# Optimization experiments

Measured on AMD Instinct MI355X. Metric: run time of the kernel, lower is better.

The kernel has to match this reference:

```python
import jax, jax.numpy as jnp
import numpy as np

B, S, D, H, F, L = 4, 2048, 768, 12, 3072, 4
DH = D // H  # dim_head = 64
EPS = 1e-5


def _layernorm(x, g, b):
    mu = jnp.mean(x, axis=-1, keepdims=True)
    var = jnp.var(x, axis=-1, keepdims=True)
    return (x - mu) * jax.lax.rsqrt(var + EPS) * g + b


def setup_inputs() -> dict:
    key = jax.random.key(0)
    ks = jax.random.split(key, 12)
    sc = 0.02
    x = jax.random.normal(ks[0], (B, S, D), dtype=jnp.float32)
    # causal mask: True where attention is disallowed (j > i)
    causal = jnp.triu(jnp.ones((S, S), dtype=bool), k=1)
    attn_mask = jnp.broadcast_to(causal, (B, S, S))
    Wq = jax.random.normal(ks[1], (L, D, D), dtype=jnp.float32) * sc
    Wk = jax.random.normal(ks[2], (L, D, D), dtype=jnp.float32) * sc
    Wv = jax.random.normal(ks[3], (L, D, D), dtype=jnp.float32) * sc
    Wo = jax.random.normal(ks[4], (L, D, D), dtype=jnp.float32) * sc
    bo = jnp.zeros((L, D), dtype=jnp.float32)
    ln1_g = jnp.ones((L, D), dtype=jnp.float32)
    ln1_b = jnp.zeros((L, D), dtype=jnp.float32)
    W1 = jax.random.normal(ks[5], (L, D, F), dtype=jnp.float32) * sc
    b1 = jnp.zeros((L, F), dtype=jnp.float32)
    W2 = jax.random.normal(ks[6], (L, F, D), dtype=jnp.float32) * sc
    b2 = jnp.zeros((L, D), dtype=jnp.float32)
    ln2_g = jnp.ones((L, D), dtype=jnp.float32)
    ln2_b = jnp.zeros((L, D), dtype=jnp.float32)
    return dict(x=x, attn_mask=attn_mask, Wq=Wq, Wk=Wk, Wv=Wv, Wo=Wo, bo=bo,
                ln1_g=ln1_g, ln1_b=ln1_b, W1=W1, b1=b1, W2=W2, b2=b2,
                ln2_g=ln2_g, ln2_b=ln2_b)


def _decoder_layer(x, mask, Wq, Wk, Wv, Wo, bo, ln1_g, ln1_b, W1, b1, W2, b2, ln2_g, ln2_b):
    # multi-head attention (dropout = identity in eval)
    q = (x @ Wq).reshape(B, S, H, DH).transpose(0, 2, 1, 3)  # (B,H,S,DH)
    k = (x @ Wk).reshape(B, S, H, DH).transpose(0, 2, 1, 3)
    v = (x @ Wv).reshape(B, S, H, DH).transpose(0, 2, 1, 3)
    a = jnp.einsum('bhqd,bhkd->bhqk', q, k) / jnp.sqrt(jnp.float32(DH))
    a = jnp.where(mask[:, None, :, :], jnp.float32(-1e9), a)
    p = jax.nn.softmax(a, axis=-1)
    av = jnp.einsum('bhqk,bhkd->bhqd', p, v)
    av = av.transpose(0, 2, 1, 3).reshape(B, S, D)
    attn_out = av @ Wo + bo
    h = _layernorm(x + attn_out, ln1_g, ln1_b)
    # FFN: Conv1d(kernel=1) == pointwise linear; exact GELU (torch F.gelu default)
    f = jax.nn.gelu(h @ W1 + b1, approximate=False) @ W2 + b2
    return _layernorm(h + f, ln2_g, ln2_b)


def reference(x, attn_mask, Wq, Wk, Wv, Wo, bo, ln1_g, ln1_b, W1, b1, W2, b2, ln2_g, ln2_b):
    for l in range(L):
        x = _decoder_layer(x, attn_mask, Wq[l], Wk[l], Wv[l], Wo[l], bo[l],
                           ln1_g[l], ln1_b[l], W1[l], b1[l], W2[l], b2[l],
                           ln2_g[l], ln2_b[l])
    return x
```

## Files before the change

kernel.cpp:

```cpp
#include <hip/hip_runtime.h>
#include <hip/hip_bf16.h>
#include <math.h>

#define BB 4
#define SS 2048
#define DD 768
#define HH 12
#define DHD 64
#define FF 3072
#define LL 4

typedef float ffrag __attribute__((ext_vector_type(4)));
typedef __bf16 bf16x8 __attribute__((ext_vector_type(8)));
typedef __bf16 bf16x4 __attribute__((ext_vector_type(4)));

__device__ __forceinline__ void gld_lds16(const __bf16* g, __bf16* l) {
  __builtin_amdgcn_global_load_lds(
      (const __attribute__((address_space(1))) void*)g,
      (__attribute__((address_space(3))) void*)l, 16, 0, 0);
}

__device__ __forceinline__ float gelu_f(float x) {
  const float x2 = x * x;
  const float e = __expf(x * fmaf(-0.0713548162f, x2, -1.5957691216f));
  return x / (1.f + e);
}

template <int SWAP>
__device__ __forceinline__ void gemm_core(
    const __bf16* __restrict__ A, const __bf16* __restrict__ Bt,
    __bf16* As, __bf16* Bs, int m0, int n0, int K, int kbeg, int kend,
    int lane, int wid, ffrag (&acc)[4][4]) {
  const int kr = lane >> 4;
  const int ml = lane & 15;
  const int wm = (wid >> 1) * 64;
  const int wn = (wid & 1) * 64;
  for (int k0 = kbeg; k0 < kend; k0 += 64) {
    __syncthreads();
#pragma unroll
    for (int it = 0; it < 4; ++it) {
      const int gidx = it * 256 + wid * 64 + lane;
      const int row = gidx >> 3;
      const int gl = (gidx & 7) ^ (row & 7);
      gld_lds16(A + (size_t)(m0 + row) * K + k0 + gl * 8,
                As + (size_t)(it * 256 + wid * 64) * 8);
      gld_lds16(Bt + (size_t)(n0 + row) * K + k0 + gl * 8,
                Bs + (size_t)(it * 256 + wid * 64) * 8);
    }
    __syncthreads();
#pragma unroll
    for (int kh = 0; kh < 2; ++kh) {
      const int gb = kh * 4 + kr;
      bf16x8 af[4], bfr[4];
#pragma unroll
      for (int i = 0; i < 4; ++i) {
        const int ra = wm + i * 16 + ml;
        af[i] = *(const bf16x8*)(As + ra * 64 + ((gb ^ (ra & 7)) * 8));
        const int rb = wn + i * 16 + ml;
        bfr[i] = *(const bf16x8*)(Bs + rb * 64 + ((gb ^ (rb & 7)) * 8));
      }
#pragma unroll
      for (int i = 0; i < 4; ++i)
#pragma unroll
        for (int j = 0; j < 4; ++j) {
          if (SWAP)
            acc[i][j] = __builtin_amdgcn_mfma_f32_16x16x32_bf16(
                bfr[j], af[i], acc[i][j], 0, 0, 0);
          else
            acc[i][j] = __builtin_amdgcn_mfma_f32_16x16x32_bf16(
                af[i], bfr[j], acc[i][j], 0, 0, 0);
        }
    }
  }
}

template <int ACT, int WRITE_BF16, int SPLITK>
__global__ __launch_bounds__(256) void gemm_std(
    const __bf16* __restrict__ A, const __bf16* __restrict__ Bt,
    const float* __restrict__ bias, float* __restrict__ Cf,
    __bf16* __restrict__ Cb, int M, int N, int K) {
  __shared__ __bf16 As[128 * 64];
  __shared__ __bf16 Bs[128 * 64];
  const int tid = threadIdx.x;
  const int lane = tid & 63;
  const int wid = tid >> 6;
  const int m0 = blockIdx.y * 128;
  const int n0 = blockIdx.x * 128;
  const int wm = (wid >> 1) * 64;
  const int wn = (wid & 1) * 64;
  const int ml = lane & 15;
  const int quad = lane >> 4;

  int kbeg = 0, kend = K;
  if (SPLITK) {
    const int z = blockIdx.z;
    const int half = K >> 1;
    kbeg = z * half;
    kend = kbeg + half;
    Cf += (size_t)z * M * N;
    if (z) bias = nullptr;
  }

  ffrag acc[4][4];
#pragma unroll
  for (int i = 0; i < 4; ++i)
#pragma unroll
    for (int j = 0; j < 4; ++j) acc[i][j] = (ffrag)0.f;

  gemm_core<1>(A, Bt, As, Bs, m0, n0, K, kbeg, kend, lane, wid, acc);

#pragma unroll
  for (int j = 0; j < 4; ++j) {
    const int ncol = n0 + wn + j * 16 + quad * 4;
    float4 b4 = make_float4(0.f, 0.f, 0.f, 0.f);
    if (bias) b4 = *(const float4*)(bias + ncol);
#pragma unroll
    for (int i = 0; i < 4; ++i) {
      const int mrow = m0 + wm + i * 16 + ml;
      float v0 = acc[i][j][0] + b4.x;
      float v1 = acc[i][j][1] + b4.y;
      float v2 = acc[i][j][2] + b4.z;
      float v3 = acc[i][j][3] + b4.w;
      if (ACT) {
        v0 = gelu_f(v0); v1 = gelu_f(v1);
        v2 = gelu_f(v2); v3 = gelu_f(v3);
      }
      if (WRITE_BF16) {
        bf16x4 pk;
        pk[0] = (__bf16)v0; pk[1] = (__bf16)v1;
        pk[2] = (__bf16)v2; pk[3] = (__bf16)v3;
        *(bf16x4*)(Cb + (size_t)mrow * N + ncol) = pk;
      } else {
        float4 o; o.x = v0; o.y = v1; o.z = v2; o.w = v3;
        *(float4*)(Cf + (size_t)mrow * N + ncol) = o;
      }
    }
  }
}

__global__ __launch_bounds__(256) void gemm_qkv(
    const __bf16* __restrict__ A, const __bf16* __restrict__ Bt,
    __bf16* __restrict__ QKb, __bf16* __restrict__ Vt, int M, int K) {
  __shared__ __bf16 As[128 * 64];
  __shared__ __bf16 Bs[128 * 64];
  const int tid = threadIdx.x;
  const int lane = tid & 63;
  const int wid = tid >> 6;
  const int m0 = blockIdx.y * 128;
  const int n0 = blockIdx.x * 128;
  const int wm = (wid >> 1) * 64;
  const int wn = (wid & 1) * 64;
  const int ml = lane & 15;
  const int quad = lane >> 4;

  ffrag acc[4][4];
#pragma unroll
  for (int i = 0; i < 4; ++i)
#pragma unroll
    for (int j = 0; j < 4; ++j) acc[i][j] = (ffrag)0.f;

  if (n0 < 1536) {
    gemm_core<1>(A, Bt, As, Bs, m0, n0, K, 0, K, lane, wid, acc);
#pragma unroll
    for (int j = 0; j < 4; ++j) {
      const int ncol = n0 + wn + j * 16 + quad * 4;
#pragma unroll
      for (int i = 0; i < 4; ++i) {
        const int mrow = m0 + wm + i * 16 + ml;
        bf16x4 pk;
#pragma unroll
        for (int r = 0; r < 4; ++r) pk[r] = (__bf16)acc[i][j][r];
        *(bf16x4*)(QKb + (size_t)mrow * 1536 + ncol) = pk;
      }
    }
  } else {
    gemm_core<0>(A, Bt, As, Bs, m0, n0, K, 0, K, lane, wid, acc);
#pragma unroll
    for (int j = 0; j < 4; ++j) {
      const int vcol = n0 - 1536 + wn + j * 16 + ml;
      const int hh = vcol >> 6, d = vcol & 63;
#pragma unroll
      for (int i = 0; i < 4; ++i) {
        const int row = m0 + wm + i * 16 + quad * 4;
        const int bi = row >> 11, s = row & 2047;
        bf16x4 pk;
#pragma unroll
        for (int r = 0; r < 4; ++r) pk[r] = (__bf16)acc[i][j][r];
        *(bf16x4*)(Vt + ((size_t)(bi * HH + hh) * DHD + d) * SS + s) = pk;
      }
    }
  }
}

__global__ __launch_bounds__(256) void wtrans_kernel(
    const float* __restrict__ src, __bf16* __restrict__ dst, int R, int C,
    size_t src_ls, size_t dst_ls) {
  __shared__ float t[32][33];
  src += (size_t)blockIdx.z * src_ls;
  dst += (size_t)blockIdx.z * dst_ls;
  const int tx = threadIdx.x & 31;
  const int ty = threadIdx.x >> 5;
  const int r0 = blockIdx.y * 32;
  const int c0 = blockIdx.x * 32;
#pragma unroll
  for (int i = 0; i < 4; ++i)
    t[ty + i * 8][tx] = src[(size_t)(r0 + ty + i * 8) * C + c0 + tx];
  __syncthreads();
#pragma unroll
  for (int i = 0; i < 4; ++i)
    dst[(size_t)(c0 + ty + i * 8) * R + r0 + tx] = (__bf16)t[tx][ty + i * 8];
}

__global__ __launch_bounds__(256) void cvt_kernel(
    const float* __restrict__ x, __bf16* __restrict__ y, int n4) {
  const int i = blockIdx.x * 256 + threadIdx.x;
  if (i < n4) {
    const float4 v = *(const float4*)(x + (size_t)i * 4);
    bf16x4 o;
    o[0] = (__bf16)v.x; o[1] = (__bf16)v.y;
    o[2] = (__bf16)v.z; o[3] = (__bf16)v.w;
    *(bf16x4*)(y + (size_t)i * 4) = o;
  }
}

__global__ __launch_bounds__(256, 3) void attn_mfma(
    const __bf16* __restrict__ QK, const __bf16* __restrict__ VT,
    __bf16* __restrict__ O) {
  __shared__ __bf16 qs[64 * 64];
  __shared__ __bf16 ks[2][64 * 64];
  __shared__ __bf16 vts[2][64 * 64];
  __shared__ __bf16 ps[64 * 72];

  const int flat = (int)blockIdx.x + 16 * ((int)blockIdx.y + 12 * (int)blockIdx.z);
  const int sw = (flat & 7) * 96 + (flat >> 3);
  const int xq = sw & 15;
  const int bh = sw >> 4;
  const int h = bh % HH;
  const int b = bh / HH;

  const int tid = threadIdx.x;
  const int lane = tid & 63;
  const int wid = tid >> 6;
  const int ml = lane & 15;
  const int quad = lane >> 4;
  const int wq = wid * 16;
  const size_t rowbase = (size_t)b * SS;
  const int hc = h * 64;
  const size_t vbase = (size_t)(b * HH + h) * DHD;
  const int NT = SS / 64;

  const int gidx0 = wid * 64 + lane;
  const int row0 = gidx0 >> 3;
  const int gl0 = (gidx0 & 7) ^ (row0 & 7);
  const int gidx1 = 256 + wid * 64 + lane;
  const int row1 = gidx1 >> 3;
  const int gl1 = (gidx1 & 7) ^ (row1 & 7);

  for (int ph = 0; ph < 2; ++ph) {
    const int qt = ph ? (NT - 1 - xq) : xq;
    const int q0 = qt * 64;

    __syncthreads();

    gld_lds16(QK + (rowbase + q0 + row0) * 1536 + hc + gl0 * 8,
              qs + (size_t)(wid * 64) * 8);
    gld_lds16(QK + (rowbase + q0 + row1) * 1536 + hc + gl1 * 8,
              qs + (size_t)(256 + wid * 64) * 8);
    gld_lds16(QK + (rowbase + row0) * 1536 + 768 + hc + gl0 * 8,
              ks[0] + (size_t)(wid * 64) * 8);
    gld_lds16(QK + (rowbase + row1) * 1536 + 768 + hc + gl1 * 8,
              ks[0] + (size_t)(256 + wid * 64) * 8);
    gld_lds16(VT + (vbase + row0) * SS + gl0 * 8, vts[0] + (size_t)(wid * 64) * 8);
    gld_lds16(VT + (vbase + row1) * SS + gl1 * 8, vts[0] + (size_t)(256 + wid * 64) * 8);

    ffrag oacc[4];
#pragma unroll
    for (int d = 0; d < 4; ++d) oacc[d] = (ffrag)0.f;
    float l_acc = 0.f;

    for (int ch = 0; ch <= qt; ++ch) {
      const int j0 = ch * 64;
      const int cur = ch & 1;
      __syncthreads();

      if (ch < qt) {
        const int jn = j0 + 64;
        gld_lds16(QK + (rowbase + jn + row0) * 1536 + 768 + hc + gl0 * 8,
                  ks[cur ^ 1] + (size_t)(wid * 64) * 8);
        gld_lds16(QK + (rowbase + jn + row1) * 1536 + 768 + hc + gl1 * 8,
                  ks[cur ^ 1] + (size_t)(256 + wid * 64) * 8);
        gld_lds16(VT + (vbase + row0) * SS + jn + gl0 * 8,
                  vts[cur ^ 1] + (size_t)(wid * 64) * 8);
        gld_lds16(VT + (vbase + row1) * SS + jn + gl1 * 8,
                  vts[cur ^ 1] + (size_t)(256 + wid * 64) * 8);
      }

      ffrag sa[4];
#pragma unroll
      for (int jt = 0; jt < 4; ++jt) sa[jt] = (ffrag)0.f;
#pragma unroll
      for (int kk = 0; kk < 2; ++kk) {
        const int gb = kk * 4 + quad;
        const int ra = wq + ml;
        const bf16x8 qf = *(const bf16x8*)(qs + ra * 64 + ((gb ^ (ra & 7)) * 8));
#pragma unroll
        for (int jt = 0; jt < 4; ++jt) {
          const int rb = jt * 16 + ml;
          const bf16x8 kf =
              *(const bf16x8*)(ks[cur] + rb * 64 + ((gb ^ (rb & 7)) * 8));
          sa[jt] = __builtin_amdgcn_mfma_f32_16x16x32_bf16(kf, qf, sa[jt], 0, 0, 0);
        }
      }

      const bool maskch = (j0 == q0);
      const int qrel = wq + ml;
      float lsum = 0.f;
      bf16x4 pk[4];
#pragma unroll
      for (int jt = 0; jt < 4; ++jt) {
#pragma unroll
        for (int r = 0; r < 4; ++r) {
          float p = __expf(sa[jt][r] * 0.125f);
          if (maskch && (jt * 16 + quad * 4 + r > qrel)) p = 0.f;
          lsum += p;
          pk[jt][r] = (__bf16)p;
        }
      }
      lsum += __shfl_xor(lsum, 16);
      lsum += __shfl_xor(lsum, 32);
      l_acc += lsum;

#pragma unroll
      for (int jt = 0; jt < 4; ++jt)
        *(bf16x4*)(ps + (size_t)(wq + ml) * 72 + jt * 16 + quad * 4) = pk[jt];

#pragma unroll
      for (int kk = 0; kk < 2; ++kk) {
        const bf16x8 ap =
            *(const bf16x8*)(ps + (size_t)(wq + ml) * 72 + kk * 32 + quad * 8);
        const int gb = kk * 4 + quad;
#pragma unroll
        for (int d = 0; d < 4; ++d) {
          const int rv = d * 16 + ml;
          const bf16x8 bv =
              *(const bf16x8*)(vts[cur] + rv * 64 + ((gb ^ (rv & 7)) * 8));
          oacc[d] = __builtin_amdgcn_mfma_f32_16x16x32_bf16(ap, bv, oacc[d], 0, 0, 0);
        }
      }
    }

#pragma unroll
    for (int r = 0; r < 4; ++r) {
      const int qloc = quad * 4 + r;
      const float lr = __shfl(l_acc, qloc);
      const float inv = 1.f / lr;
      const size_t row = rowbase + q0 + wq + qloc;
#pragma unroll
      for (int d = 0; d < 4; ++d)
        O[row * DD + hc + d * 16 + ml] = (__bf16)(oacc[d][r] * inv);
    }
  }
}

__global__ __launch_bounds__(256) void add_ln_kernel(
    const __bf16* __restrict__ X, const float* __restrict__ R1,
    const float* __restrict__ R2, const float* __restrict__ g,
    const float* __restrict__ be, float* __restrict__ Ofp,
    __bf16* __restrict__ Ob) {
  const int row = blockIdx.x * 4 + (threadIdx.x >> 6);
  const int lane = threadIdx.x & 63;
  const __bf16* xr = X + (size_t)row * DD;
  const float* r1 = R1 + (size_t)row * DD;
  const float* r2 = R2 ? R2 + (size_t)row * DD : nullptr;
  float v[12];
  float sum = 0.f;
#pragma unroll
  for (int i = 0; i < 3; ++i) {
    const int c = i * 256 + lane * 4;
    const bf16x4 a = *(const bf16x4*)(xr + c);
    const float4 b = *(const float4*)(r1 + c);
    float4 c2 = make_float4(0.f, 0.f, 0.f, 0.f);
    if (r2) c2 = *(const float4*)(r2 + c);
    v[i * 4 + 0] = (float)a[0] + b.x + c2.x;
    v[i * 4 + 1] = (float)a[1] + b.y + c2.y;
    v[i * 4 + 2] = (float)a[2] + b.z + c2.z;
    v[i * 4 + 3] = (float)a[3] + b.w + c2.w;
    sum += v[i * 4 + 0] + v[i * 4 + 1] + v[i * 4 + 2] + v[i * 4 + 3];
  }
#pragma unroll
  for (int off = 32; off >= 1; off >>= 1) sum += __shfl_xor(sum, off);
  const float mean = sum * (1.f / 768.f);
  float sq = 0.f;
#pragma unroll
  for (int i = 0; i < 12; ++i) {
    const float d = v[i] - mean;
    sq += d * d;
  }
#pragma unroll
  for (int off = 32; off >= 1; off >>= 1) sq += __shfl_xor(sq, off);
  const float inv = rsqrtf(sq * (1.f / 768.f) + 1e-5f);
#pragma unroll
  for (int i = 0; i < 3; ++i) {
    const int c = i * 256 + lane * 4;
    const float4 gg = *(const float4*)(g + c);
    const float4 bb = *(const float4*)(be + c);
    float4 o;
    o.x = (v[i * 4 + 0] - mean) * inv * gg.x + bb.x;
    o.y = (v[i * 4 + 1] - mean) * inv * gg.y + bb.y;
    o.z = (v[i * 4 + 2] - mean) * inv * gg.z + bb.z;
    o.w = (v[i * 4 + 3] - mean) * inv * gg.w + bb.w;
    if (Ofp) *(float4*)(Ofp + (size_t)row * DD + c) = o;
    if (Ob) {
      bf16x4 ob;
      ob[0] = (__bf16)o.x; ob[1] = (__bf16)o.y;
      ob[2] = (__bf16)o.z; ob[3] = (__bf16)o.w;
      *(bf16x4*)(Ob + (size_t)row * DD + c) = ob;
    }
  }
}

extern "C" void kernel_launch(void* const* d_in, const int* in_sizes, int n_in,
                              void* d_out, int out_size, void* d_ws,
                              size_t ws_size, hipStream_t stream) {
  const float* x0   = (const float*)d_in[0];
  const float* Wq   = (const float*)d_in[2];
  const float* Wk   = (const float*)d_in[3];
  const float* Wv   = (const float*)d_in[4];
  const float* Wo   = (const float*)d_in[5];
  const float* bo   = (const float*)d_in[6];
  const float* ln1g = (const float*)d_in[7];
  const float* ln1b = (const float*)d_in[8];
  const float* W1   = (const float*)d_in[9];
  const float* b1   = (const float*)d_in[10];
  const float* W2   = (const float*)d_in[11];
  const float* b2   = (const float*)d_in[12];
  const float* ln2g = (const float*)d_in[13];
  const float* ln2b = (const float*)d_in[14];

  float* out = (float*)d_out;

  const size_t NTD = (size_t)BB * SS * DD;
  __bf16* qkbf = (__bf16*)d_ws;
  __bf16* vtbf = qkbf + (size_t)BB * SS * 1536;
  __bf16* btbf = vtbf + NTD;
  __bf16* midbf = qkbf;
  __bf16* hbf  = btbf + NTD;
  float* aw    = (float*)(hbf + NTD);
  __bf16* wT   = (__bf16*)(aw + 2 * NTD);
  __bf16* xbf  = (__bf16*)d_out;

  const size_t WTL = 7077888;
  const size_t OQK = 0, OWO = (size_t)2304 * 768, OW1 = 2359296, OW2 = 4718592;

  const int M = BB * SS;
  const size_t DSQ = (size_t)DD * DD;

  cvt_kernel<<<(int)(NTD / 4 + 255) / 256, 256, 0, stream>>>(x0, xbf, (int)(NTD / 4));

  wtrans_kernel<<<dim3(24, 24, LL), 256, 0, stream>>>(Wq, wT + OQK, DD, DD, DSQ, WTL);
  wtrans_kernel<<<dim3(24, 24, LL), 256, 0, stream>>>(Wk, wT + (size_t)768 * 768, DD, DD, DSQ, WTL);
  wtrans_kernel<<<dim3(24, 24, LL), 256, 0, stream>>>(Wv, wT + (size_t)1536 * 768, DD, DD, DSQ, WTL);
  wtrans_kernel<<<dim3(24, 24, LL), 256, 0, stream>>>(Wo, wT + OWO, DD, DD, DSQ, WTL);
  wtrans_kernel<<<dim3(96, 24, LL), 256, 0, stream>>>(W1, wT + OW1, DD, FF, (size_t)DD * FF, WTL);
  wtrans_kernel<<<dim3(24, 96, LL), 256, 0, stream>>>(W2, wT + OW2, FF, DD, (size_t)FF * DD, WTL);

  for (int l = 0; l < LL; ++l) {
    const float* bol = bo + (size_t)l * DD;
    const float* g1 = ln1g + (size_t)l * DD;
    const float* be1 = ln1b + (size_t)l * DD;
    const float* b1l = b1 + (size_t)l * FF;
    const float* b2l = b2 + (size_t)l * DD;
    const float* g2 = ln2g + (size_t)l * DD;
    const float* be2 = ln2b + (size_t)l * DD;
    __bf16* wqkvT = wT + l * WTL + OQK;
    __bf16* woT   = wT + l * WTL + OWO;
    __bf16* w1T   = wT + l * WTL + OW1;
    __bf16* w2T   = wT + l * WTL + OW2;
    const bool last = (l == LL - 1);

    gemm_qkv<<<dim3(18, 64), 256, 0, stream>>>(xbf, wqkvT, qkbf, vtbf, M, DD);
    attn_mfma<<<dim3(SS / 128, HH, BB), 256, 0, stream>>>(qkbf, vtbf, btbf);
    gemm_std<0, 0, 0><<<dim3(6, 64), 256, 0, stream>>>(
        btbf, woT, bol, aw, nullptr, M, DD, DD);
    add_ln_kernel<<<M / 4, 256, 0, stream>>>(
        xbf, aw, nullptr, g1, be1, nullptr, hbf);
    gemm_std<1, 1, 0><<<dim3(24, 64), 256, 0, stream>>>(
        hbf, w1T, b1l, nullptr, midbf, M, FF, DD);
    gemm_std<0, 0, 1><<<dim3(6, 64, 2), 256, 0, stream>>>(
        midbf, w2T, b2l, aw, nullptr, M, DD, FF);
    add_ln_kernel<<<M / 4, 256, 0, stream>>>(
        hbf, aw, aw + NTD, g2, be2, last ? out : nullptr, last ? nullptr : xbf);
  }
}
```

Measured before the change: 1.208 ms.

## Add triple-buffered 256x128 FFN1 GEMM and XCD-aware block swizzle

Adds a new 512-thread GEMM kernel for the FFN up-projection with 256x128 tiles and a three-stage LDS pipeline driven by explicit vmcnt waits. It uses direct global-to-LDS loads and raises MFMA priority during compute, aiming to hide load latency. All GEMMs also remap block indices so neighbouring tiles land on the same XCD, which should improve L2 reuse. The larger LDS footprint (about 144KB) may limit occupancy to one block per CU.

```diff
diff --git a/kernel.cpp b/kernel.cpp
--- a/kernel.cpp
+++ b/kernel.cpp
@@ -24,6 +24,10 @@
   const float x2 = x * x;
   const float e = __expf(x * fmaf(-0.0713548162f, x2, -1.5957691216f));
   return x / (1.f + e);
+}
+
+__device__ __forceinline__ int xcd_swz(int flat, int nwg) {
+  return (flat & 7) * (nwg >> 3) + (flat >> 3);
 }
 
 template <int SWAP>
@@ -84,8 +88,13 @@
   const int tid = threadIdx.x;
   const int lane = tid & 63;
   const int wid = tid >> 6;
-  const int m0 = blockIdx.y * 128;
-  const int n0 = blockIdx.x * 128;
+  const int nx = (int)gridDim.x, ny = (int)gridDim.y, nz = (int)gridDim.z;
+  const int flat = (int)blockIdx.x + nx * ((int)blockIdx.y + ny * (int)blockIdx.z);
+  const int sw = xcd_swz(flat, nx * ny * nz);
+  const int m0 = (sw % ny) * 128;
+  const int r = sw / ny;
+  const int n0 = (r % nx) * 128;
+  const int z = r / nx;
   const int wm = (wid >> 1) * 64;
   const int wn = (wid & 1) * 64;
   const int ml = lane & 15;
@@ -93,7 +102,6 @@
 
   int kbeg = 0, kend = K;
   if (SPLITK) {
-    const int z = blockIdx.z;
     const int half = K >> 1;
     kbeg = z * half;
     kend = kbeg + half;
@@ -138,6 +146,122 @@
   }
 }
 
+__device__ __forceinline__ void stage3(const __bf16* A, const __bf16* Bt,
+                                       __bf16* as, __bf16* bs, int K, int k0,
+                                       int tid, int wid) {
+#pragma unroll
+  for (int it = 0; it < 4; ++it) {
+    const int gidx = it * 512 + tid;
+    const int row = gidx >> 3;
+    const int gl = (gidx & 7) ^ (row & 7);
+    gld_lds16(A + (size_t)row * K + k0 + gl * 8,
+              as + (size_t)(it * 512 + wid * 64) * 8);
+  }
+#pragma unroll
+  for (int it = 0; it < 2; ++it) {
+    const int gidx = it * 512 + tid;
+    const int row = gidx >> 3;
+    const int gl = (gidx & 7) ^ (row & 7);
+    gld_lds16(Bt + (size_t)row * K + k0 + gl * 8,
+              bs + (size_t)(it * 512 + wid * 64) * 8);
+  }
+}
+
+template <int ACT>
+__global__ __launch_bounds__(512) void gemm3s(
+    const __bf16* __restrict__ A, const __bf16* __restrict__ Bt,
+    const float* __restrict__ bias, __bf16* __restrict__ Cb,
+    int M, int N, int K) {
+  __shared__ __bf16 As[3][256 * 64];
+  __shared__ __bf16 Bs[3][128 * 64];
+  const int tid = threadIdx.x;
+  const int lane = tid & 63;
+  const int wid = tid >> 6;
+  const int nx = N >> 7;
+  const int ny = M >> 8;
+  const int flat = (int)blockIdx.x + nx * (int)blockIdx.y;
+  const int sw = xcd_swz(flat, nx * ny);
+  const int m0 = (sw % ny) * 256;
+  const int n0 = (sw / ny) * 128;
+  const __bf16* Ab = A + (size_t)m0 * K;
+  const __bf16* Bb = Bt + (size_t)n0 * K;
+  const int ml = lane & 15;
+  const int kr = lane >> 4;
+  const int quad = kr;
+  const int wm = (wid >> 1) * 64;
+  const int wn = (wid & 1) * 64;
+
+  ffrag acc[4][4];
+#pragma unroll
+  for (int i = 0; i < 4; ++i)
+#pragma unroll
+    for (int j = 0; j < 4; ++j) acc[i][j] = (ffrag)0.f;
+
+  const int nt = K >> 6;
+  stage3(Ab, Bb, As[0], Bs[0], K, 0, tid, wid);
+  if (nt > 1) stage3(Ab, Bb, As[1], Bs[1], K, 64, tid, wid);
+
+  for (int t = 0; t < nt; ++t) {
+    const int s = t % 3;
+    if (t + 2 < nt)
+      stage3(Ab, Bb, As[(t + 2) % 3], Bs[(t + 2) % 3], K, (t + 2) * 64, tid, wid);
+    if (t + 2 < nt)
+      asm volatile("s_waitcnt vmcnt(12)" ::: "memory");
+    else if (t + 1 < nt)
+      asm volatile("s_waitcnt vmcnt(6)" ::: "memory");
+    else
+      asm volatile("s_waitcnt vmcnt(0)" ::: "memory");
+    __builtin_amdgcn_s_barrier();
+    const __bf16* as = As[s];
+    const __bf16* bs = Bs[s];
+#pragma unroll
+    for (int kh = 0; kh < 2; ++kh) {
+      const int gb = kh * 4 + kr;
+      bf16x8 af[4], bfr[4];
+#pragma unroll
+      for (int i = 0; i < 4; ++i) {
+        const int ra = wm + i * 16 + ml;
+        af[i] = *(const bf16x8*)(as + ra * 64 + ((gb ^ (ra & 7)) * 8));
+        const int rb = wn + i * 16 + ml;
+        bfr[i] = *(const bf16x8*)(bs + rb * 64 + ((gb ^ (rb & 7)) * 8));
+      }
+      __builtin_amdgcn_s_setprio(1);
+#pragma unroll
+      for (int i = 0; i < 4; ++i)
+#pragma unroll
+        for (int j = 0; j < 4; ++j)
+          acc[i][j] = __builtin_amdgcn_mfma_f32_16x16x32_bf16(
+              bfr[j], af[i], acc[i][j], 0, 0, 0);
+      __builtin_amdgcn_s_setprio(0);
+    }
+    asm volatile("s_waitcnt lgkmcnt(0)" ::: "memory");
+    __builtin_amdgcn_s_barrier();
+  }
+
+#pragma unroll
+  for (int j = 0; j < 4; ++j) {
+    const int ncol = n0 + wn + j * 16 + quad * 4;
+    float4 b4 = make_float4(0.f, 0.f, 0.f, 0.f);
+    if (bias) b4 = *(const float4*)(bias + ncol);
+#pragma unroll
+    for (int i = 0; i < 4; ++i) {
+      const int mrow = m0 + wm + i * 16 + ml;
+      float v0 = acc[i][j][0] + b4.x;
+      float v1 = acc[i][j][1] + b4.y;
+      float v2 = acc[i][j][2] + b4.z;
+      float v3 = acc[i][j][3] + b4.w;
+      if (ACT) {
+        v0 = gelu_f(v0); v1 = gelu_f(v1);
+        v2 = gelu_f(v2); v3 = gelu_f(v3);
+      }
+      bf16x4 pk;
+      pk[0] = (__bf16)v0; pk[1] = (__bf16)v1;
+      pk[2] = (__bf16)v2; pk[3] = (__bf16)v3;
+      *(bf16x4*)(Cb + (size_t)mrow * N + ncol) = pk;
+    }
+  }
+}
+
 __global__ __launch_bounds__(256) void gemm_qkv(
     const __bf16* __restrict__ A, const __bf16* __restrict__ Bt,
     __bf16* __restrict__ QKb, __bf16* __restrict__ Vt, int M, int K) {
@@ -146,8 +270,11 @@
   const int tid = threadIdx.x;
   const int lane = tid & 63;
   const int wid = tid >> 6;
-  const int m0 = blockIdx.y * 128;
-  const int n0 = blockIdx.x * 128;
+  const int nx = (int)gridDim.x, ny = (int)gridDim.y;
+  const int flat = (int)blockIdx.x + nx * (int)blockIdx.y;
+  const int sw = xcd_swz(flat, nx * ny);
+  const int m0 = (sw % ny) * 128;
+  const int n0 = (sw / ny) * 128;
   const int wm = (wid >> 1) * 64;
   const int wn = (wid & 1) * 64;
   const int ml = lane & 15;
@@ -484,8 +611,8 @@
         btbf, woT, bol, aw, nullptr, M, DD, DD);
     add_ln_kernel<<<M / 4, 256, 0, stream>>>(
         xbf, aw, nullptr, g1, be1, nullptr, hbf);
-    gemm_std<1, 1, 0><<<dim3(24, 64), 256, 0, stream>>>(
-        hbf, w1T, b1l, nullptr, midbf, M, FF, DD);
+    gemm3s<1><<<dim3(FF / 128, M / 256), 512, 0, stream>>>(
+        hbf, w1T, b1l, midbf, M, FF, DD);
     gemm_std<0, 0, 1><<<dim3(6, 64, 2), 256, 0, stream>>>(
         midbf, w2T, b2l, aw, nullptr, M, DD, FF);
     add_ln_kernel<<<M / 4, 256, 0, stream>>>(
```

Result: slower. 1.319 ms (+9.1%).

## Double-buffer GEMM LDS tiles, raise MFMA priority, swizzle blocks across XCDs

Applied to the files above, without the earlier changes.

The GEMM core now double-buffers its shared-memory tiles. It issues the global-to-LDS loads for the next K tile before running the MFMAs on the current one, which removes the second barrier per iteration and overlaps load latency with compute. MFMA sections are wrapped in s_setprio, and the block index is remapped with an XCD-aware swizzle so neighbouring tiles land on the same XCD and share its L2. In exchange, LDS use per block doubles to 64KB, which can lower occupancy.

```diff
diff --git a/kernel.cpp b/kernel.cpp
--- a/kernel.cpp
+++ b/kernel.cpp
@@ -24,6 +24,26 @@
   const float x2 = x * x;
   const float e = __expf(x * fmaf(-0.0713548162f, x2, -1.5957691216f));
   return x / (1.f + e);
+}
+
+__device__ __forceinline__ int xcd_swz(int flat, int nwg) {
+  return (flat & 7) * (nwg >> 3) + (flat >> 3);
+}
+
+__device__ __forceinline__ void stage_tile(
+    const __bf16* __restrict__ A, const __bf16* __restrict__ Bt,
+    __bf16* As, __bf16* Bs, int m0, int n0, int K, int k0,
+    int lane, int wid) {
+#pragma unroll
+  for (int it = 0; it < 4; ++it) {
+    const int gidx = it * 256 + wid * 64 + lane;
+    const int row = gidx >> 3;
+    const int gl = (gidx & 7) ^ (row & 7);
+    gld_lds16(A + (size_t)(m0 + row) * K + k0 + gl * 8,
+              As + (size_t)(it * 256 + wid * 64) * 8);
+    gld_lds16(Bt + (size_t)(n0 + row) * K + k0 + gl * 8,
+              Bs + (size_t)(it * 256 + wid * 64) * 8);
+  }
 }
 
 template <int SWAP>
@@ -35,19 +55,16 @@
   const int ml = lane & 15;
   const int wm = (wid >> 1) * 64;
   const int wn = (wid & 1) * 64;
+
+  stage_tile(A, Bt, As, Bs, m0, n0, K, kbeg, lane, wid);
+  int cur = 0;
   for (int k0 = kbeg; k0 < kend; k0 += 64) {
     __syncthreads();
-#pragma unroll
-    for (int it = 0; it < 4; ++it) {
-      const int gidx = it * 256 + wid * 64 + lane;
-      const int row = gidx >> 3;
-      const int gl = (gidx & 7) ^ (row & 7);
-      gld_lds16(A + (size_t)(m0 + row) * K + k0 + gl * 8,
-                As + (size_t)(it * 256 + wid * 64) * 8);
-      gld_lds16(Bt + (size_t)(n0 + row) * K + k0 + gl * 8,
-                Bs + (size_t)(it * 256 + wid * 64) * 8);
-    }
-    __syncthreads();
+    if (k0 + 64 < kend)
+      stage_tile(A, Bt, As + (cur ^ 1) * 8192, Bs + (cur ^ 1) * 8192,
+                 m0, n0, K, k0 + 64, lane, wid);
+    const __bf16* as = As + cur * 8192;
+    const __bf16* bs = Bs + cur * 8192;
 #pragma unroll
     for (int kh = 0; kh < 2; ++kh) {
       const int gb = kh * 4 + kr;
@@ -55,10 +72,11 @@
 #pragma unroll
       for (int i = 0; i < 4; ++i) {
         const int ra = wm + i * 16 + ml;
-        af[i] = *(const bf16x8*)(As + ra * 64 + ((gb ^ (ra & 7)) * 8));
+        af[i] = *(const bf16x8*)(as + ra * 64 + ((gb ^ (ra & 7)) * 8));
         const int rb = wn + i * 16 + ml;
-        bfr[i] = *(const bf16x8*)(Bs + rb * 64 + ((gb ^ (rb & 7)) * 8));
-      }
+        bfr[i] = *(const bf16x8*)(bs + rb * 64 + ((gb ^ (rb & 7)) * 8));
+      }
+      __builtin_amdgcn_s_setprio(1);
 #pragma unroll
       for (int i = 0; i < 4; ++i)
 #pragma unroll
@@ -70,7 +88,9 @@
             acc[i][j] = __builtin_amdgcn_mfma_f32_16x16x32_bf16(
                 af[i], bfr[j], acc[i][j], 0, 0, 0);
         }
-    }
+      __builtin_amdgcn_s_setprio(0);
+    }
+    cur ^= 1;
   }
 }
 
@@ -79,13 +99,18 @@
     const __bf16* __restrict__ A, const __bf16* __restrict__ Bt,
     const float* __restrict__ bias, float* __restrict__ Cf,
     __bf16* __restrict__ Cb, int M, int N, int K) {
-  __shared__ __bf16 As[128 * 64];
-  __shared__ __bf16 Bs[128 * 64];
+  __shared__ __bf16 As[2 * 128 * 64];
+  __shared__ __bf16 Bs[2 * 128 * 64];
   const int tid = threadIdx.x;
   const int lane = tid & 63;
   const int wid = tid >> 6;
-  const int m0 = blockIdx.y * 128;
-  const int n0 = blockIdx.x * 128;
+  const int nx = (int)gridDim.x, ny = (int)gridDim.y, nz = (int)gridDim.z;
+  const int flat = (int)blockIdx.x + nx * ((int)blockIdx.y + ny * (int)blockIdx.z);
+  const int sw = xcd_swz(flat, nx * ny * nz);
+  const int m0 = (sw % ny) * 128;
+  const int r = sw / ny;
+  const int n0 = (r % nx) * 128;
+  const int z = r / nx;
   const int wm = (wid >> 1) * 64;
   const int wn = (wid & 1) * 64;
   const int ml = lane & 15;
@@ -93,7 +118,6 @@
 
   int kbeg = 0, kend = K;
   if (SPLITK) {
-    const int z = blockIdx.z;
     const int half = K >> 1;
     kbeg = z * half;
     kend = kbeg + half;
@@ -141,13 +165,16 @@
 __global__ __launch_bounds__(256) void gemm_qkv(
     const __bf16* __restrict__ A, const __bf16* __restrict__ Bt,
     __bf16* __restrict__ QKb, __bf16* __restrict__ Vt, int M, int K) {
-  __shared__ __bf16 As[128 * 64];
-  __shared__ __bf16 Bs[128 * 64];
+  __shared__ __bf16 As[2 * 128 * 64];
+  __shared__ __bf16 Bs[2 * 128 * 64];
   const int tid = threadIdx.x;
   const int lane = tid & 63;
   const int wid = tid >> 6;
-  const int m0 = blockIdx.y * 128;
-  const int n0 = blockIdx.x * 128;
+  const int nx = (int)gridDim.x, ny = (int)gridDim.y;
+  const int flat = (int)blockIdx.x + nx * (int)blockIdx.y;
+  const int sw = xcd_swz(flat, nx * ny);
+  const int m0 = (sw % ny) * 128;
+  const int n0 = (sw / ny) * 128;
   const int wm = (wid >> 1) * 64;
   const int wn = (wid & 1) * 64;
   const int ml = lane & 15;
```

New measurement: 1.357 ms. +12.4%, slower.
